# Performance work log

Hardware: AMD Instinct MI355X
Metric: run time of the kernel (lower is better)

The kernel has to match this reference:

```python
import jax, jax.numpy as jnp
import numpy as np

D = 128
HIDDEN = 512
N = 2048


def setup_inputs() -> dict:
    key = jax.random.key(0)
    k_x, k0, k1, k2 = jax.random.split(key, 4)
    x = jax.random.normal(k_x, (N, D), dtype=jnp.float32)
    # LocallyConnected init: uniform(-sqrt(1/in), sqrt(1/in))
    b0 = 1.0 / np.sqrt(D)
    b1 = 1.0 / np.sqrt(HIDDEN)
    W0 = jax.random.uniform(k0, (D, D, HIDDEN), jnp.float32, -b0, b0)
    W1 = jax.random.uniform(k1, (D, HIDDEN, HIDDEN), jnp.float32, -b1, b1)
    W2 = jax.random.uniform(k2, (D, HIDDEN, 1), jnp.float32, -b1, b1)
    return {"x": x, "W0": W0, "W1": W1, "W2": W2}


def reference(x, W0, W1, W2):
    n, d = x.shape
    # masking layer: matmul with diag(mask[i]) == elementwise zero-out of diagonal
    mask = 1.0 - jnp.eye(d, dtype=x.dtype)          # [d, d]
    h = x[:, None, :] * mask[None, :, :]            # [n, d, d]
    # per-node locally-connected MLP
    h = jax.nn.leaky_relu(jnp.einsum('ndi,dio->ndo', h, W0))   # [n, d, hidden]
    h = jax.nn.leaky_relu(jnp.einsum('ndi,dio->ndo', h, W1))   # [n, d, hidden]
    h = jnp.einsum('ndi,dio->ndo', h, W2)                      # [n, d, 1]
    return h.squeeze(-1)                                       # [n, d]
```

## Files before the change

kernel.cpp:

```cpp
#include <hip/hip_runtime.h>

#define DD 128
#define HH 512
#define NN 2048
#define NT 64
#define XS_LD 136
#define H1_LD 520

typedef __bf16 bf16x8 __attribute__((ext_vector_type(8)));
typedef __bf16 bf16x4 __attribute__((ext_vector_type(4)));
typedef float  floatx4 __attribute__((ext_vector_type(4)));

__global__ void pack_w(const float* __restrict__ W, __bf16* __restrict__ Wp,
                       int K, int ks_log2, int total) {
    int t = blockIdx.x * blockDim.x + threadIdx.x;
    if (t >= total) return;
    int c     = t & 15;
    int q     = (t >> 4) & 3;
    int rest  = t >> 6;
    int nks_m = (K >> 5) - 1;
    int ks    = rest & nks_m;
    int rest2 = rest >> ks_log2;
    int ct    = rest2 & 31;
    int d     = rest2 >> 5;
    int col   = ct * 16 + c;
    const float* src = W + ((size_t)d * K + ks * 32 + q * 8) * HH + col;
    bf16x8 v;
#pragma unroll
    for (int j = 0; j < 8; j++) v[j] = (__bf16)src[(size_t)j * HH];
    *(bf16x8*)(Wp + (size_t)t * 8) = v;
}

__launch_bounds__(512, 2)
__global__ void grandag_main(const float* __restrict__ x,
                             const __bf16* __restrict__ W0p,
                             const __bf16* __restrict__ W1p,
                             const float* __restrict__ W2,
                             float* __restrict__ out) {
    __shared__ __bf16 Xs[NT * XS_LD];
    __shared__ __bf16 h1s[NT * H1_LD];
    __shared__ float  outp[NT];

    const int b  = blockIdx.x;
    const int d  = ((b >> 8) << 3) | (b & 7);
    const int t  = (b >> 3) & 31;
    const int n0 = t * NT;

    const int tid = threadIdx.x;
    const int w   = tid >> 6;
    const int l   = tid & 63;
    const int lc  = l & 15;
    const int lq  = l >> 4;

#pragma unroll
    for (int it = 0; it < 4; it++) {
        int e  = (tid + it * 512) * 4;
        int rr = e >> 7;
        int i  = e & 127;
        float4 v = *(const float4*)(x + (size_t)(n0 + rr) * DD + i);
        bf16x4 o;
        o[0] = (i + 0 == d) ? (__bf16)0.f : (__bf16)v.x;
        o[1] = (i + 1 == d) ? (__bf16)0.f : (__bf16)v.y;
        o[2] = (i + 2 == d) ? (__bf16)0.f : (__bf16)v.z;
        o[3] = (i + 3 == d) ? (__bf16)0.f : (__bf16)v.w;
        *(bf16x4*)(Xs + rr * XS_LD + i) = o;
    }
    if (tid < NT) outp[tid] = 0.f;
    __syncthreads();

    {
        floatx4 acc[4][4] = {};
        bf16x8 af[2][4], bfm[2][4];
        auto loadA = [&](bf16x8* a, int ks) {
#pragma unroll
            for (int rt = 0; rt < 4; rt++)
                a[rt] = *(const bf16x8*)(Xs + (16 * rt + lc) * XS_LD + ks * 32 + lq * 8);
        };
        auto loadB = [&](bf16x8* bb, int ks) {
#pragma unroll
            for (int ct = 0; ct < 4; ct++)
                bb[ct] = *(const bf16x8*)(W0p +
                    ((((size_t)d * 32 + (w * 4 + ct)) * 4 + ks) * 64 + lq * 16 + lc) * 8);
        };
        loadA(af[0], 0); loadB(bfm[0], 0);
#pragma unroll
        for (int ks = 0; ks < 4; ks++) {
            if (ks < 3) { loadA(af[(ks + 1) & 1], ks + 1); loadB(bfm[(ks + 1) & 1], ks + 1); }
#pragma unroll
            for (int rt = 0; rt < 4; rt++)
#pragma unroll
                for (int ct = 0; ct < 4; ct++)
                    acc[rt][ct] = __builtin_amdgcn_mfma_f32_16x16x32_bf16(
                        af[ks & 1][rt], bfm[ks & 1][ct], acc[rt][ct], 0, 0, 0);
        }
#pragma unroll
        for (int rt = 0; rt < 4; rt++)
#pragma unroll
            for (int ct = 0; ct < 4; ct++)
#pragma unroll
                for (int g = 0; g < 4; g++) {
                    float v = acc[rt][ct][g];
                    v = v > 0.f ? v : 0.01f * v;
                    h1s[(16 * rt + lq * 4 + g) * H1_LD + w * 64 + 16 * ct + lc] = (__bf16)v;
                }
    }
    __syncthreads();

    floatx4 acc2[4][4] = {};
    {
        bf16x8 af[2][4], bfm[2][4];
        auto loadA = [&](bf16x8* a, int ks) {
#pragma unroll
            for (int rt = 0; rt < 4; rt++)
                a[rt] = *(const bf16x8*)(h1s + (16 * rt + lc) * H1_LD + ks * 32 + lq * 8);
        };
        auto loadB = [&](bf16x8* bb, int ks) {
#pragma unroll
            for (int ct = 0; ct < 4; ct++)
                bb[ct] = *(const bf16x8*)(W1p +
                    ((((size_t)d * 32 + (w * 4 + ct)) * 16 + ks) * 64 + lq * 16 + lc) * 8);
        };
        loadA(af[0], 0); loadB(bfm[0], 0);
#pragma unroll
        for (int ks = 0; ks < 16; ks++) {
            if (ks < 15) { loadA(af[(ks + 1) & 1], ks + 1); loadB(bfm[(ks + 1) & 1], ks + 1); }
#pragma unroll
            for (int rt = 0; rt < 4; rt++)
#pragma unroll
                for (int ct = 0; ct < 4; ct++)
                    acc2[rt][ct] = __builtin_amdgcn_mfma_f32_16x16x32_bf16(
                        af[ks & 1][rt], bfm[ks & 1][ct], acc2[rt][ct], 0, 0, 0);
        }
    }

    float w2v[4];
#pragma unroll
    for (int ct = 0; ct < 4; ct++)
        w2v[ct] = W2[(size_t)d * HH + w * 64 + 16 * ct + lc];
#pragma unroll
    for (int rt = 0; rt < 4; rt++)
#pragma unroll
        for (int g = 0; g < 4; g++) {
            float s = 0.f;
#pragma unroll
            for (int ct = 0; ct < 4; ct++) {
                float v = acc2[rt][ct][g];
                v = v > 0.f ? v : 0.01f * v;
                s += v * w2v[ct];
            }
            s += __shfl_xor(s, 1, 64);
            s += __shfl_xor(s, 2, 64);
            s += __shfl_xor(s, 4, 64);
            s += __shfl_xor(s, 8, 64);
            if (lc == 0) atomicAdd(&outp[16 * rt + lq * 4 + g], s);
        }
    __syncthreads();
    if (tid < NT) out[(size_t)(n0 + tid) * DD + d] = outp[tid];
}

extern "C" void kernel_launch(void* const* d_in, const int* in_sizes, int n_in,
                              void* d_out, int out_size, void* d_ws, size_t ws_size,
                              hipStream_t stream) {
    const float* x  = (const float*)d_in[0];
    const float* W0 = (const float*)d_in[1];
    const float* W1 = (const float*)d_in[2];
    const float* W2 = (const float*)d_in[3];
    float* out = (float*)d_out;

    __bf16* W0p = (__bf16*)d_ws;
    __bf16* W1p = (__bf16*)((char*)d_ws + (size_t)DD * DD * HH * 2);

    const int tot0 = DD * DD * HH / 8;
    const int tot1 = DD * HH * HH / 8;
    pack_w<<<dim3(tot0 / 256), 256, 0, stream>>>(W0, W0p, DD, 2, tot0);
    pack_w<<<dim3(tot1 / 256), 256, 0, stream>>>(W1, W1p, HH, 4, tot1);

    grandag_main<<<dim3(DD * (NN / NT)), 512, 0, stream>>>(x, W0p, W1p, W2, out);
}
```

Before: 455.6 us.

## Stage weight packing through LDS and read pre-converted bf16 x from global

The weight pack kernel now loads contiguous 32-row slabs into LDS with coalesced float4 reads and transposes from there, replacing the old strided per-element global gathers. x is converted to bf16 once in a separate kernel. The main kernel reads A fragments straight from global, applying the diagonal mask in registers, and drops the Xs LDS buffer and one barrier. The launch bound is raised to 4 blocks per CU. The smaller LDS footprint may allow higher occupancy, but the tighter launch bound may cause register spills given the large accumulator arrays.

```diff
diff --git a/kernel.cpp b/kernel.cpp
--- a/kernel.cpp
+++ b/kernel.cpp
@@ -4,40 +4,58 @@
 #define HH 512
 #define NN 2048
 #define NT 64
-#define XS_LD 136
 #define H1_LD 520
+#define PLD 516
 
 typedef __bf16 bf16x8 __attribute__((ext_vector_type(8)));
 typedef __bf16 bf16x4 __attribute__((ext_vector_type(4)));
 typedef float  floatx4 __attribute__((ext_vector_type(4)));
 
-__global__ void pack_w(const float* __restrict__ W, __bf16* __restrict__ Wp,
-                       int K, int ks_log2, int total) {
+__global__ void cvt_x(const float* __restrict__ x, __bf16* __restrict__ xb) {
     int t = blockIdx.x * blockDim.x + threadIdx.x;
-    if (t >= total) return;
-    int c     = t & 15;
-    int q     = (t >> 4) & 3;
-    int rest  = t >> 6;
-    int nks_m = (K >> 5) - 1;
-    int ks    = rest & nks_m;
-    int rest2 = rest >> ks_log2;
-    int ct    = rest2 & 31;
-    int d     = rest2 >> 5;
-    int col   = ct * 16 + c;
-    const float* src = W + ((size_t)d * K + ks * 32 + q * 8) * HH + col;
-    bf16x8 v;
-#pragma unroll
-    for (int j = 0; j < 8; j++) v[j] = (__bf16)src[(size_t)j * HH];
-    *(bf16x8*)(Wp + (size_t)t * 8) = v;
+    float4 v = *(const float4*)(x + (size_t)t * 4);
+    bf16x4 o;
+    o[0] = (__bf16)v.x; o[1] = (__bf16)v.y; o[2] = (__bf16)v.z; o[3] = (__bf16)v.w;
+    *(bf16x4*)(xb + (size_t)t * 4) = o;
 }
 
-__launch_bounds__(512, 2)
-__global__ void grandag_main(const float* __restrict__ x,
+__global__ void pack_w(const float* __restrict__ W, __bf16* __restrict__ Wp, int nks) {
+    __shared__ __bf16 Ls[32 * PLD];
+    const int d  = blockIdx.x / nks;
+    const int ks = blockIdx.x % nks;
+    const int tid = threadIdx.x;
+    const float* src = W + ((size_t)(d * nks + ks) * 32) * HH;
+
+#pragma unroll
+    for (int it = 0; it < 16; ++it) {
+        int e = (it * 256 + tid) * 4;
+        float4 v = *(const float4*)(src + e);
+        bf16x4 o;
+        o[0] = (__bf16)v.x; o[1] = (__bf16)v.y; o[2] = (__bf16)v.z; o[3] = (__bf16)v.w;
+        *(bf16x4*)(Ls + (e >> 9) * PLD + (e & 511)) = o;
+    }
+    __syncthreads();
+
+#pragma unroll
+    for (int it = 0; it < 8; ++it) {
+        int ch = it * 256 + tid;
+        int c  = ch & 15;
+        int q  = (ch >> 4) & 3;
+        int ct = ch >> 6;
+        bf16x8 v;
+#pragma unroll
+        for (int j = 0; j < 8; ++j)
+            v[j] = Ls[(q * 8 + j) * PLD + ct * 16 + c];
+        *(bf16x8*)(Wp + ((size_t)(d * 32 + ct) * nks + ks) * 512 + (ch & 63) * 8) = v;
+    }
+}
+
+__launch_bounds__(512, 4)
+__global__ void grandag_main(const __bf16* __restrict__ xb,
                              const __bf16* __restrict__ W0p,
                              const __bf16* __restrict__ W1p,
                              const float* __restrict__ W2,
                              float* __restrict__ out) {
-    __shared__ __bf16 Xs[NT * XS_LD];
     __shared__ __bf16 h1s[NT * H1_LD];
     __shared__ float  outp[NT];
 
@@ -52,21 +70,11 @@
     const int lc  = l & 15;
     const int lq  = l >> 4;
 
-#pragma unroll
-    for (int it = 0; it < 4; it++) {
-        int e  = (tid + it * 512) * 4;
-        int rr = e >> 7;
-        int i  = e & 127;
-        float4 v = *(const float4*)(x + (size_t)(n0 + rr) * DD + i);
-        bf16x4 o;
-        o[0] = (i + 0 == d) ? (__bf16)0.f : (__bf16)v.x;
-        o[1] = (i + 1 == d) ? (__bf16)0.f : (__bf16)v.y;
-        o[2] = (i + 2 == d) ? (__bf16)0.f : (__bf16)v.z;
-        o[3] = (i + 3 == d) ? (__bf16)0.f : (__bf16)v.w;
-        *(bf16x4*)(Xs + rr * XS_LD + i) = o;
-    }
+    const int ksz = d >> 5;
+    const int lqz = (d >> 3) & 3;
+    const int jz  = d & 7;
+
     if (tid < NT) outp[tid] = 0.f;
-    __syncthreads();
 
     {
         floatx4 acc[4][4] = {};
@@ -74,7 +82,14 @@
         auto loadA = [&](bf16x8* a, int ks) {
 #pragma unroll
             for (int rt = 0; rt < 4; rt++)
-                a[rt] = *(const bf16x8*)(Xs + (16 * rt + lc) * XS_LD + ks * 32 + lq * 8);
+                a[rt] = *(const bf16x8*)(xb + (size_t)(n0 + 16 * rt + lc) * DD + ks * 32 + lq * 8);
+            if (ks == ksz && lq == lqz) {
+#pragma unroll
+                for (int rt = 0; rt < 4; rt++)
+#pragma unroll
+                    for (int j = 0; j < 8; j++)
+                        if (j == jz) a[rt][j] = (__bf16)0.f;
+            }
         };
         auto loadB = [&](bf16x8* bb, int ks) {
 #pragma unroll
@@ -169,11 +184,12 @@
 
     __bf16* W0p = (__bf16*)d_ws;
     __bf16* W1p = (__bf16*)((char*)d_ws + (size_t)DD * DD * HH * 2);
+    __bf16* xb  = (__bf16*)((char*)d_ws + (size_t)DD * DD * HH * 2
+                                        + (size_t)DD * HH * HH * 2);
 
-    const int tot0 = DD * DD * HH / 8;
-    const int tot1 = DD * HH * HH / 8;
-    pack_w<<<dim3(tot0 / 256), 256, 0, stream>>>(W0, W0p, DD, 2, tot0);
-    pack_w<<<dim3(tot1 / 256), 256, 0, stream>>>(W1, W1p, HH, 4, tot1);
+    cvt_x<<<dim3(NN * DD / (256 * 4)), 256, 0, stream>>>(x, xb);
+    pack_w<<<dim3(DD * (DD / 32)), 256, 0, stream>>>(W0, W0p, DD / 32);
+    pack_w<<<dim3(DD * (HH / 32)), 256, 0, stream>>>(W1, W1p, HH / 32);
 
-    grandag_main<<<dim3(DD * (NN / NT)), 512, 0, stream>>>(x, W0p, W1p, W2, out);
+    grandag_main<<<dim3(DD * (NN / NT)), 512, 0, stream>>>(xb, W0p, W1p, W2, out);
 }
```

Result: slower. 506.7 us (+11.2%).
